# Kernel optimization log

Hardware: AMD Instinct MI355X
Metric: run time of the kernel (lower is better)

Reference implementation:

```python
import jax, jax.numpy as jnp
import numpy as np
from jax import lax

SIGMA = 5
RADIUS = int(4 * SIGMA + 0.5)  # 20 -> kernel size 41, pad_size = 41//2 = 20 = RADIUS
D_AP = 2.27
D_DV = 2.27


def _gauss_d1_kernel():
    # gaussian_kernel1d(sigma, order=1, radius): q(x) = -x/sigma^2, kernel = q(x)*phi(x)
    x = np.arange(-RADIUS, RADIUS + 1).astype(np.float64)
    phi = np.exp(-0.5 / SIGMA ** 2 * x ** 2)
    phi = phi / phi.sum()
    return ((-x / SIGMA ** 2) * phi).astype(np.float32)

_KERNEL = jnp.asarray(_gauss_d1_kernel())


def _conv1d_valid(x, k):
    # x: [N, L], k: [K] -> [N, L-K+1]; cross-correlation, same as torch F.conv1d
    return lax.conv_general_dilated(x[:, None, :], k[None, None, :], (1,), 'VALID')[:, 0, :]


def diffY(x):
    # circular padding along H, derivative / dDV
    c, h, w = x.shape
    xp = jnp.pad(x, ((0, 0), (RADIUS, RADIUS), (0, 0)), mode='wrap')
    xp = jnp.transpose(xp, (0, 2, 1)).reshape(c * w, h + 2 * RADIUS)
    out = _conv1d_valid(xp, _KERNEL).reshape(c, w, h)
    return jnp.transpose(out, (0, 2, 1)) / D_DV


def diffX(x):
    # reflect padding along W, derivative / dAP
    c, h, w = x.shape
    xp = jnp.pad(x, ((0, 0), (0, 0), (RADIUS, RADIUS)), mode='reflect')
    out = _conv1d_valid(xp.reshape(c * h, w + 2 * RADIUS), _KERNEL).reshape(c, h, w)
    return out / D_AP


def setup_inputs() -> dict:
    key = jax.random.key(0)
    k1, k2, k3, k4, k5 = jax.random.split(key, 5)
    H, W = 1024, 2048
    return {
        'y': jax.random.normal(k1, (5, H, W), dtype=jnp.float32),
        'v': jax.random.normal(k2, (2, H, W), dtype=jnp.float32),
        'gamma_ds': jax.random.normal(k3, (H, W), dtype=jnp.float32),
        'cad_coefs': jax.random.uniform(k4, (3,), dtype=jnp.float32),
        'myo_coefs': jax.random.uniform(k5, (5,), dtype=jnp.float32),
    }


def reference(y, v, gamma_ds, cad_coefs, myo_coefs):
    H, W = y.shape[-2:]
    m4 = y[:4]                                  # [4,H,W] myosin components
    c1 = y[4:]                                  # [1,H,W] cadherin

    d1_m = jnp.stack([diffY(m4), diffX(m4)], axis=-1).reshape(2, 2, H, W, 2)
    m = m4.reshape(2, 2, H, W)
    d1_c = jnp.stack([diffY(c1), diffX(c1)], axis=-1).reshape(H, W, 2)
    c = c1[0]

    d1_v = jnp.stack([diffY(v), diffX(v)], axis=-1)   # [2,H,W,2]: d1_v[i,y,x,j] = d_j v_i
    gv = jnp.einsum('iyxj->ijyx', d1_v)
    gvT = jnp.einsum('jyxi->ijyx', d1_v)
    O = -0.5 * (gv - gvT)                       # vorticity
    E = 0.5 * (gv + gvT)                        # strain rate

    eye = jnp.eye(2, dtype=y.dtype)[:, :, None, None]
    trm_yx = jnp.einsum('kkyx->yx', m)
    deviatoric = m - 0.5 * trm_yx[None, None] * eye

    m_norm = jnp.sqrt(jnp.sum(m * m, axis=(0, 1), keepdims=True))            # [1,1,H,W]
    m_0 = jnp.mean(m_norm, axis=(2, 3), keepdims=True)                       # [1,1,1,1]
    dev_mag = jnp.sqrt(jnp.sum(deviatoric * deviatoric, axis=(0, 1), keepdims=True))
    devE = jnp.einsum('klyx,klyx->yx', deviatoric, E)[None, None]

    E_active = E - jnp.sign(devE) * devE * deviatoric / dev_mag ** 2
    E_active = 0.5 * E_active * dev_mag / m_0
    E_passive = E - E_active

    mE = (jnp.einsum('ikyx,kjyx->ijyx', m, E_passive)
          + jnp.einsum('ikyx,kjyx->ijyx', E_passive, m))

    cad = jax.nn.relu(cad_coefs)
    myo = jax.nn.relu(myo_coefs)

    cdot = (-jnp.einsum('iyx,yxi->yx', v, d1_c)
            - cad[0] * c
            + cad[1] * c * jnp.einsum('iyxi->yx', d1_v)
            + cad[2] * gamma_ds)

    trm = trm_yx[None, None]
    gamma_dv = jnp.array([[1.0, 0.0], [0.0, 0.0]], dtype=y.dtype)[:, :, None, None]

    mdot = (-jnp.einsum('kyx,ijyxk->ijyx', v, d1_m)
            - jnp.einsum('ikyx,kjyx->ijyx', O, m)
            + jnp.einsum('ikyx,kjyx->ijyx', m, O)
            - myo[0] * m
            + myo[1] * mE
            - myo[2] * c[None, None] * mE
            + myo[3] * trm * gamma_dv
            + myo[4] * trm * m)

    return jnp.concatenate([mdot.reshape(4, H, W), cdot[None]], axis=0)
```

## Files before the change

kernel.cpp:

```cpp
#include <hip/hip_runtime.h>
#include <math.h>

#define RAD 20
#define KLEN 41
#define NH 1024
#define NW 2048
#define NHW (NH * NW)

struct KW { float w[KLEN]; };
constexpr double cexp_neg(double u) {
  double term = 1.0, sum = 1.0;
  for (int k = 1; k < 30; ++k) { term *= (-u) / (double)k; sum += term; }
  return sum;
}
constexpr KW make_kw() {
  KW r{};
  double ph[KLEN] = {};
  double s = 0.0;
  for (int i = 0; i < KLEN; ++i) {
    double d = (double)(i - RAD);
    double e = cexp_neg(d * d / 800.0);
    e = e * e; e = e * e; e = e * e; e = e * e;
    ph[i] = e; s += e;
  }
  for (int i = 0; i < KLEN; ++i) {
    double d = (double)(i - RAD);
    r.w[i] = (float)((-d / 25.0) * (ph[i] / s) / 2.27);
  }
  return r;
}
static constexpr KW KWC = make_kw();

template <int K>
__device__ __forceinline__ void tap(float s, float& r0, float& r1, float& r2,
                                    float& r3, float& r4, float& r5, float& r6,
                                    float& r7) {
  if constexpr (K - 0 >= 0 && K - 0 <= 40) r0 = fmaf(s, KWC.w[K - 0], r0);
  if constexpr (K - 1 >= 0 && K - 1 <= 40) r1 = fmaf(s, KWC.w[K - 1], r1);
  if constexpr (K - 2 >= 0 && K - 2 <= 40) r2 = fmaf(s, KWC.w[K - 2], r2);
  if constexpr (K - 3 >= 0 && K - 3 <= 40) r3 = fmaf(s, KWC.w[K - 3], r3);
  if constexpr (K - 4 >= 0 && K - 4 <= 40) r4 = fmaf(s, KWC.w[K - 4], r4);
  if constexpr (K - 5 >= 0 && K - 5 <= 40) r5 = fmaf(s, KWC.w[K - 5], r5);
  if constexpr (K - 6 >= 0 && K - 6 <= 40) r6 = fmaf(s, KWC.w[K - 6], r6);
  if constexpr (K - 7 >= 0 && K - 7 <= 40) r7 = fmaf(s, KWC.w[K - 7], r7);
}

#define R8 r0, r1, r2, r3, r4, r5, r6, r7

#define TW 64
#define TH 32
#define TILE_CH ((TH + 2 * RAD) * TW)

__device__ __forceinline__ void conv_col(const float* __restrict__ t, int base,
                                         int lane, float& r0, float& r1,
                                         float& r2, float& r3, float& r4,
                                         float& r5, float& r6, float& r7) {
#define CCHUNK(c)                                      \
  {                                                    \
    float s0 = t[(base + 4 * (c) + 0) * TW + lane];    \
    float s1 = t[(base + 4 * (c) + 1) * TW + lane];    \
    float s2 = t[(base + 4 * (c) + 2) * TW + lane];    \
    float s3 = t[(base + 4 * (c) + 3) * TW + lane];    \
    tap<4 * (c) + 0>(s0, R8);                          \
    tap<4 * (c) + 1>(s1, R8);                          \
    tap<4 * (c) + 2>(s2, R8);                          \
    tap<4 * (c) + 3>(s3, R8);                          \
  }
  CCHUNK(0) CCHUNK(1) CCHUNK(2) CCHUNK(3) CCHUNK(4) CCHUNK(5)
  CCHUNK(6) CCHUNK(7) CCHUNK(8) CCHUNK(9) CCHUNK(10) CCHUNK(11)
#undef CCHUNK
}

__global__ __launch_bounds__(256) void k_reduce(const float* __restrict__ y,
                                                double* __restrict__ acc) {
  const int tid = blockIdx.x * blockDim.x + threadIdx.x;
  const int stride = gridDim.x * blockDim.x;
  double local = 0.0;
  for (int q = tid; q < NHW / 4; q += stride) {
    float4 a = ((const float4*)y)[q];
    float4 b = ((const float4*)(y + NHW))[q];
    float4 c = ((const float4*)(y + 2 * (size_t)NHW))[q];
    float4 d = ((const float4*)(y + 3 * (size_t)NHW))[q];
    local += (double)sqrtf(a.x * a.x + b.x * b.x + c.x * c.x + d.x * d.x);
    local += (double)sqrtf(a.y * a.y + b.y * b.y + c.y * c.y + d.y * d.y);
    local += (double)sqrtf(a.z * a.z + b.z * b.z + c.z * c.z + d.z * d.z);
    local += (double)sqrtf(a.w * a.w + b.w * b.w + c.w * c.w + d.w * d.w);
  }
#pragma unroll
  for (int off = 32; off > 0; off >>= 1) local += __shfl_down(local, off, 64);
  __shared__ double smem[4];
  const int lane = threadIdx.x & 63;
  const int wid = threadIdx.x >> 6;
  if (lane == 0) smem[wid] = local;
  __syncthreads();
  if (threadIdx.x == 0) {
    double s = smem[0] + smem[1] + smem[2] + smem[3];
    atomicAdd(acc, s);
  }
}

__global__ __launch_bounds__(256) void k_dx(const float* __restrict__ y,
                                            const float* __restrict__ v,
                                            float* __restrict__ ws) {
  __shared__ float row[2120];
  const int t = threadIdx.x;
  const int r = blockIdx.x;
  const int ch = blockIdx.y;
  const float* src = (ch < 5) ? (y + (size_t)ch * NHW) : (v + (size_t)(ch - 5) * NHW);
  const float* rp = src + (size_t)r * NW;

#define SWZ(i) ((i) + ((i) >> 6))
#define ST(i, val) { const int ii_ = (i); row[SWZ(ii_)] = (val); }

  const float4* rp4 = (const float4*)rp;
  float4 b0 = rp4[t];
  float4 b1 = rp4[t + 256];
  ST(RAD + 4 * t + 0, b0.x)
  ST(RAD + 4 * t + 1, b0.y)
  ST(RAD + 4 * t + 2, b0.z)
  ST(RAD + 4 * t + 3, b0.w)
  ST(RAD + 4 * (t + 256) + 0, b1.x)
  ST(RAD + 4 * (t + 256) + 1, b1.y)
  ST(RAD + 4 * (t + 256) + 2, b1.z)
  ST(RAD + 4 * (t + 256) + 3, b1.w)
  if (t < RAD) {
    ST(t, rp[RAD - t])
    ST(NW + RAD + t, rp[NW - 2 - t])
  }
  __syncthreads();

  const int xb = 8 * t;
  float r0 = 0.f, r1 = 0.f, r2 = 0.f, r3 = 0.f;
  float r4 = 0.f, r5 = 0.f, r6 = 0.f, r7 = 0.f;
#define RD(k) { const int x_ = xb + (k); float s_ = row[SWZ(x_)]; tap<(k)>(s_, R8); }
  RD(0)  RD(1)  RD(2)  RD(3)  RD(4)  RD(5)  RD(6)  RD(7)
  RD(8)  RD(9)  RD(10) RD(11) RD(12) RD(13) RD(14) RD(15)
  RD(16) RD(17) RD(18) RD(19) RD(20) RD(21) RD(22) RD(23)
  RD(24) RD(25) RD(26) RD(27) RD(28) RD(29) RD(30) RD(31)
  RD(32) RD(33) RD(34) RD(35) RD(36) RD(37) RD(38) RD(39)
  RD(40) RD(41) RD(42) RD(43) RD(44) RD(45) RD(46) RD(47)
#undef RD

  float4 o0, o1;
  o0.x = r0; o0.y = r1; o0.z = r2; o0.w = r3;
  o1.x = r4; o1.y = r5; o1.z = r6; o1.w = r7;
  float4* dst = (float4*)(ws + (size_t)(7 + ch) * NHW + (size_t)r * NW + xb);
  dst[0] = o0;
  dst[1] = o1;
}

__global__ __launch_bounds__(256, 4) void k_dyf(
    const float* __restrict__ y, const float* __restrict__ v,
    const float* __restrict__ gds, const float* __restrict__ cadc,
    const float* __restrict__ myoc, const float* __restrict__ ws,
    const double* __restrict__ acc, float* __restrict__ out) {
  __shared__ float tile[2 * TILE_CH];
  const int lane = threadIdx.x & 63;
  const int wid = threadIdx.x >> 6;
  const int x0 = blockIdx.x * TW;
  const int yb = blockIdx.y * TH;
  const int base = wid * 8;

  const float m0 = (float)(acc[0] / (double)NHW);
  const float cad0 = fmaxf(cadc[0], 0.f);
  const float cad1 = fmaxf(cadc[1], 0.f);
  const float cad2 = fmaxf(cadc[2], 0.f);
  const float my0 = fmaxf(myoc[0], 0.f);
  const float my1 = fmaxf(myoc[1], 0.f);
  const float my2 = fmaxf(myoc[2], 0.f);
  const float my3 = fmaxf(myoc[3], 0.f);
  const float my4 = fmaxf(myoc[4], 0.f);

#define SGLD(sp, k) \
  (sp)[(size_t)(((yb - RAD + wid + 4 * (k)) + NH) & (NH - 1)) * NW + x0 + lane]

  float u0, u1, u2, u3, u4, u5, u6, u7, u8;
  float u9, u10, u11, u12, u13, u14, u15, u16, u17;

#define LOADCH(srcp)                                                   \
  {                                                                    \
    const float* sp_ = (srcp);                                         \
    u0 = SGLD(sp_, 0); u1 = SGLD(sp_, 1); u2 = SGLD(sp_, 2);           \
    u3 = SGLD(sp_, 3); u4 = SGLD(sp_, 4); u5 = SGLD(sp_, 5);           \
    u6 = SGLD(sp_, 6); u7 = SGLD(sp_, 7); u8 = SGLD(sp_, 8);           \
    u9 = SGLD(sp_, 9); u10 = SGLD(sp_, 10); u11 = SGLD(sp_, 11);       \
    u12 = SGLD(sp_, 12); u13 = SGLD(sp_, 13); u14 = SGLD(sp_, 14);     \
    u15 = SGLD(sp_, 15); u16 = SGLD(sp_, 16); u17 = SGLD(sp_, 17);     \
  }
#define WRITECH(g)                                                        \
  {                                                                       \
    float* tb_ = &tile[(g) * TILE_CH];                                    \
    tb_[(wid + 0) * TW + lane] = u0;   tb_[(wid + 4) * TW + lane] = u1;   \
    tb_[(wid + 8) * TW + lane] = u2;   tb_[(wid + 12) * TW + lane] = u3;  \
    tb_[(wid + 16) * TW + lane] = u4;  tb_[(wid + 20) * TW + lane] = u5;  \
    tb_[(wid + 24) * TW + lane] = u6;  tb_[(wid + 28) * TW + lane] = u7;  \
    tb_[(wid + 32) * TW + lane] = u8;  tb_[(wid + 36) * TW + lane] = u9;  \
    tb_[(wid + 40) * TW + lane] = u10; tb_[(wid + 44) * TW + lane] = u11; \
    tb_[(wid + 48) * TW + lane] = u12; tb_[(wid + 52) * TW + lane] = u13; \
    tb_[(wid + 56) * TW + lane] = u14; tb_[(wid + 60) * TW + lane] = u15; \
    tb_[(wid + 64) * TW + lane] = u16; tb_[(wid + 68) * TW + lane] = u17; \
  }
#define DECL8(P)                                                       \
  float P##0 = 0.f, P##1 = 0.f, P##2 = 0.f, P##3 = 0.f, P##4 = 0.f,    \
        P##5 = 0.f, P##6 = 0.f, P##7 = 0.f;
#define CALLCONV(g, P)                                                  \
  conv_col(&tile[(g) * TILE_CH], base, lane, P##0, P##1, P##2, P##3,    \
           P##4, P##5, P##6, P##7);

  DECL8(ym00) DECL8(ym01) DECL8(ym10) DECL8(ym11)
  DECL8(yc) DECL8(yv0) DECL8(yv1)

  LOADCH(y)
  WRITECH(0)
  __syncthreads();
  LOADCH(y + (size_t)NHW)
  CALLCONV(0, ym00)
  WRITECH(1)
  __syncthreads();
  LOADCH(y + 2 * (size_t)NHW)
  CALLCONV(1, ym01)
  WRITECH(0)
  __syncthreads();
  LOADCH(y + 3 * (size_t)NHW)
  CALLCONV(0, ym10)
  WRITECH(1)
  __syncthreads();
  LOADCH(y + 4 * (size_t)NHW)
  CALLCONV(1, ym11)
  WRITECH(0)
  __syncthreads();
  LOADCH(v)
  CALLCONV(0, yc)
  WRITECH(1)
  __syncthreads();
  LOADCH(v + (size_t)NHW)
  CALLCONV(1, yv0)
  WRITECH(0)
  __syncthreads();
  CALLCONV(0, yv1)

#define POINT(q)                                                              \
  {                                                                           \
    const size_t idx = (size_t)(yb + base + (q)) * NW + x0 + lane;            \
    const float m00 = y[idx];                                                 \
    const float m01 = y[idx + (size_t)NHW];                                   \
    const float m10 = y[idx + 2 * (size_t)NHW];                               \
    const float m11 = y[idx + 3 * (size_t)NHW];                               \
    const float c = y[idx + 4 * (size_t)NHW];                                 \
    const float v0 = v[idx];                                                  \
    const float v1 = v[idx + (size_t)NHW];                                    \
    const float g = gds[idx];                                                 \
    const float dY_m00 = ym00##q, dY_m01 = ym01##q;                           \
    const float dY_m10 = ym10##q, dY_m11 = ym11##q;                           \
    const float dY_c = yc##q, dY_v0 = yv0##q, dY_v1 = yv1##q;                 \
    const float dX_m00 = ws[idx + 7 * (size_t)NHW];                           \
    const float dX_m01 = ws[idx + 8 * (size_t)NHW];                           \
    const float dX_m10 = ws[idx + 9 * (size_t)NHW];                           \
    const float dX_m11 = ws[idx + 10 * (size_t)NHW];                          \
    const float dX_c = ws[idx + 11 * (size_t)NHW];                            \
    const float dX_v0 = ws[idx + 12 * (size_t)NHW];                           \
    const float dX_v1 = ws[idx + 13 * (size_t)NHW];                           \
    const float gv00 = dY_v0, gv01 = dX_v0, gv10 = dY_v1, gv11 = dX_v1;       \
    const float ww = -0.5f * (gv01 - gv10);                                   \
    const float E00 = gv00, E11 = gv11;                                       \
    const float E01 = 0.5f * (gv01 + gv10);                                   \
    const float E10 = E01;                                                    \
    const float trm = m00 + m11;                                              \
    const float dev00 = m00 - 0.5f * trm;                                     \
    const float dev01 = m01;                                                  \
    const float dev10 = m10;                                                  \
    const float dev11 = m11 - 0.5f * trm;                                     \
    const float dmag_sq =                                                     \
        dev00 * dev00 + dev01 * dev01 + dev10 * dev10 + dev11 * dev11;        \
    const float dm = sqrtf(dmag_sq);                                          \
    const float dm2 = dm * dm;                                                \
    const float devE = dev00 * E00 + dev01 * E01 + dev10 * E10 + dev11 * E11; \
    const float sg = (devE > 0.f) ? 1.f : ((devE < 0.f) ? -1.f : 0.f);        \
    const float coef = sg * devE / dm2;                                       \
    const float sc = 0.5f * dm / m0;                                          \
    const float Ea00 = (E00 - coef * dev00) * sc;                             \
    const float Ea01 = (E01 - coef * dev01) * sc;                             \
    const float Ea10 = (E10 - coef * dev10) * sc;                             \
    const float Ea11 = (E11 - coef * dev11) * sc;                             \
    const float Ep00 = E00 - Ea00;                                            \
    const float Ep01 = E01 - Ea01;                                            \
    const float Ep10 = E10 - Ea10;                                            \
    const float Ep11 = E11 - Ea11;                                            \
    const float mE00 = (m00 * Ep00 + m01 * Ep10) + (Ep00 * m00 + Ep01 * m10); \
    const float mE01 = (m00 * Ep01 + m01 * Ep11) + (Ep00 * m01 + Ep01 * m11); \
    const float mE10 = (m10 * Ep00 + m11 * Ep10) + (Ep10 * m00 + Ep11 * m10); \
    const float mE11 = (m10 * Ep01 + m11 * Ep11) + (Ep10 * m01 + Ep11 * m11); \
    const float divv = gv00 + gv11;                                           \
    const float cdot =                                                        \
        -(v0 * dY_c + v1 * dX_c) - cad0 * c + cad1 * c * divv + cad2 * g;     \
    const float md00 = -(v0 * dY_m00 + v1 * dX_m00) - ww * m10 - ww * m01 -   \
                       my0 * m00 + my1 * mE00 - my2 * c * mE00 + my3 * trm +  \
                       my4 * trm * m00;                                       \
    const float md01 = -(v0 * dY_m01 + v1 * dX_m01) - ww * m11 + ww * m00 -   \
                       my0 * m01 + my1 * mE01 - my2 * c * mE01 +              \
                       my4 * trm * m01;                                       \
    const float md10 = -(v0 * dY_m10 + v1 * dX_m10) + ww * m00 - ww * m11 -   \
                       my0 * m10 + my1 * mE10 - my2 * c * mE10 +              \
                       my4 * trm * m10;                                       \
    const float md11 = -(v0 * dY_m11 + v1 * dX_m11) + ww * m01 + ww * m10 -   \
                       my0 * m11 + my1 * mE11 - my2 * c * mE11 +              \
                       my4 * trm * m11;                                       \
    out[idx] = md00;                                                          \
    out[idx + (size_t)NHW] = md01;                                            \
    out[idx + 2 * (size_t)NHW] = md10;                                        \
    out[idx + 3 * (size_t)NHW] = md11;                                        \
    out[idx + 4 * (size_t)NHW] = cdot;                                        \
  }

  POINT(0) POINT(1) POINT(2) POINT(3)
  POINT(4) POINT(5) POINT(6) POINT(7)
#undef POINT
}

extern "C" void kernel_launch(void* const* d_in, const int* in_sizes, int n_in,
                              void* d_out, int out_size, void* d_ws, size_t ws_size,
                              hipStream_t stream) {
  (void)in_sizes; (void)n_in; (void)out_size; (void)ws_size;
  const float* y = (const float*)d_in[0];
  const float* v = (const float*)d_in[1];
  const float* gds = (const float*)d_in[2];
  const float* cadc = (const float*)d_in[3];
  const float* myoc = (const float*)d_in[4];
  float* out = (float*)d_out;

  double* acc = (double*)d_ws;
  float* planes = (float*)((char*)d_ws + 512);

  hipMemsetAsync(acc, 0, sizeof(double), stream);
  k_reduce<<<dim3(1024), dim3(256), 0, stream>>>(y, acc);
  k_dx<<<dim3(NH, 7), dim3(256), 0, stream>>>(y, v, planes);
  k_dyf<<<dim3(NW / TW, NH / TH), dim3(256), 0, stream>>>(y, v, gds, cadc, myoc,
                                                          planes, acc, out);
}
```

Baseline: 179.6 us.

## Fuse myosin-magnitude reduction into dx kernel and vectorize dy tile loads

Removes the separate k_reduce launch. The channel-0 blocks of k_dx now load the other three myosin rows and compute the sqrt-magnitude reduction, reusing the row already in registers. Separately, k_dyf's halo tile load is changed from scalar per-lane loads to float4 loads and stores spread across the block. The fusion adds load imbalance: channel-0 blocks do four times the reads plus an extra barrier and atomic. The float4 tile writes may change the LDS bank pattern.

```diff
diff --git a/kernel.cpp b/kernel.cpp
--- a/kernel.cpp
+++ b/kernel.cpp
@@ -71,38 +71,12 @@
 #undef CCHUNK
 }
 
-__global__ __launch_bounds__(256) void k_reduce(const float* __restrict__ y,
-                                                double* __restrict__ acc) {
-  const int tid = blockIdx.x * blockDim.x + threadIdx.x;
-  const int stride = gridDim.x * blockDim.x;
-  double local = 0.0;
-  for (int q = tid; q < NHW / 4; q += stride) {
-    float4 a = ((const float4*)y)[q];
-    float4 b = ((const float4*)(y + NHW))[q];
-    float4 c = ((const float4*)(y + 2 * (size_t)NHW))[q];
-    float4 d = ((const float4*)(y + 3 * (size_t)NHW))[q];
-    local += (double)sqrtf(a.x * a.x + b.x * b.x + c.x * c.x + d.x * d.x);
-    local += (double)sqrtf(a.y * a.y + b.y * b.y + c.y * c.y + d.y * d.y);
-    local += (double)sqrtf(a.z * a.z + b.z * b.z + c.z * c.z + d.z * d.z);
-    local += (double)sqrtf(a.w * a.w + b.w * b.w + c.w * c.w + d.w * d.w);
-  }
-#pragma unroll
-  for (int off = 32; off > 0; off >>= 1) local += __shfl_down(local, off, 64);
-  __shared__ double smem[4];
-  const int lane = threadIdx.x & 63;
-  const int wid = threadIdx.x >> 6;
-  if (lane == 0) smem[wid] = local;
-  __syncthreads();
-  if (threadIdx.x == 0) {
-    double s = smem[0] + smem[1] + smem[2] + smem[3];
-    atomicAdd(acc, s);
-  }
-}
-
 __global__ __launch_bounds__(256) void k_dx(const float* __restrict__ y,
                                             const float* __restrict__ v,
-                                            float* __restrict__ ws) {
+                                            float* __restrict__ ws,
+                                            double* __restrict__ acc) {
   __shared__ float row[2120];
+  __shared__ double rsm[4];
   const int t = threadIdx.x;
   const int r = blockIdx.x;
   const int ch = blockIdx.y;
@@ -115,6 +89,17 @@
   const float4* rp4 = (const float4*)rp;
   float4 b0 = rp4[t];
   float4 b1 = rp4[t + 256];
+
+  float4 a1x, a1y, a2x, a2y, a3x, a3y;
+  if (ch == 0) {
+    const float4* p1 = (const float4*)(y + (size_t)NHW + (size_t)r * NW);
+    const float4* p2 = (const float4*)(y + 2 * (size_t)NHW + (size_t)r * NW);
+    const float4* p3 = (const float4*)(y + 3 * (size_t)NHW + (size_t)r * NW);
+    a1x = p1[t]; a1y = p1[t + 256];
+    a2x = p2[t]; a2y = p2[t + 256];
+    a3x = p3[t]; a3y = p3[t + 256];
+  }
+
   ST(RAD + 4 * t + 0, b0.x)
   ST(RAD + 4 * t + 1, b0.y)
   ST(RAD + 4 * t + 2, b0.z)
@@ -147,6 +132,25 @@
   float4* dst = (float4*)(ws + (size_t)(7 + ch) * NHW + (size_t)r * NW + xb);
   dst[0] = o0;
   dst[1] = o1;
+
+  if (ch == 0) {
+    double local =
+        (double)sqrtf(b0.x * b0.x + a1x.x * a1x.x + a2x.x * a2x.x + a3x.x * a3x.x) +
+        (double)sqrtf(b0.y * b0.y + a1x.y * a1x.y + a2x.y * a2x.y + a3x.y * a3x.y) +
+        (double)sqrtf(b0.z * b0.z + a1x.z * a1x.z + a2x.z * a2x.z + a3x.z * a3x.z) +
+        (double)sqrtf(b0.w * b0.w + a1x.w * a1x.w + a2x.w * a2x.w + a3x.w * a3x.w) +
+        (double)sqrtf(b1.x * b1.x + a1y.x * a1y.x + a2y.x * a2y.x + a3y.x * a3y.x) +
+        (double)sqrtf(b1.y * b1.y + a1y.y * a1y.y + a2y.y * a2y.y + a3y.y * a3y.y) +
+        (double)sqrtf(b1.z * b1.z + a1y.z * a1y.z + a2y.z * a2y.z + a3y.z * a3y.z) +
+        (double)sqrtf(b1.w * b1.w + a1y.w * a1y.w + a2y.w * a2y.w + a3y.w * a3y.w);
+#pragma unroll
+    for (int off = 32; off > 0; off >>= 1) local += __shfl_down(local, off, 64);
+    const int lane = t & 63;
+    const int wid = t >> 6;
+    if (lane == 0) rsm[wid] = local;
+    __syncthreads();
+    if (t == 0) atomicAdd(acc, rsm[0] + rsm[1] + rsm[2] + rsm[3]);
+  }
 }
 
 __global__ __launch_bounds__(256, 4) void k_dyf(
@@ -157,6 +161,7 @@
   __shared__ float tile[2 * TILE_CH];
   const int lane = threadIdx.x & 63;
   const int wid = threadIdx.x >> 6;
+  const int t = threadIdx.x;
   const int x0 = blockIdx.x * TW;
   const int yb = blockIdx.y * TH;
   const int base = wid * 8;
@@ -171,34 +176,34 @@
   const float my3 = fmaxf(myoc[3], 0.f);
   const float my4 = fmaxf(myoc[4], 0.f);
 
-#define SGLD(sp, k) \
-  (sp)[(size_t)(((yb - RAD + wid + 4 * (k)) + NH) & (NH - 1)) * NW + x0 + lane]
-
-  float u0, u1, u2, u3, u4, u5, u6, u7, u8;
-  float u9, u10, u11, u12, u13, u14, u15, u16, u17;
-
-#define LOADCH(srcp)                                                   \
-  {                                                                    \
-    const float* sp_ = (srcp);                                         \
-    u0 = SGLD(sp_, 0); u1 = SGLD(sp_, 1); u2 = SGLD(sp_, 2);           \
-    u3 = SGLD(sp_, 3); u4 = SGLD(sp_, 4); u5 = SGLD(sp_, 5);           \
-    u6 = SGLD(sp_, 6); u7 = SGLD(sp_, 7); u8 = SGLD(sp_, 8);           \
-    u9 = SGLD(sp_, 9); u10 = SGLD(sp_, 10); u11 = SGLD(sp_, 11);       \
-    u12 = SGLD(sp_, 12); u13 = SGLD(sp_, 13); u14 = SGLD(sp_, 14);     \
-    u15 = SGLD(sp_, 15); u16 = SGLD(sp_, 16); u17 = SGLD(sp_, 17);     \
-  }
-#define WRITECH(g)                                                        \
-  {                                                                       \
-    float* tb_ = &tile[(g) * TILE_CH];                                    \
-    tb_[(wid + 0) * TW + lane] = u0;   tb_[(wid + 4) * TW + lane] = u1;   \
-    tb_[(wid + 8) * TW + lane] = u2;   tb_[(wid + 12) * TW + lane] = u3;  \
-    tb_[(wid + 16) * TW + lane] = u4;  tb_[(wid + 20) * TW + lane] = u5;  \
-    tb_[(wid + 24) * TW + lane] = u6;  tb_[(wid + 28) * TW + lane] = u7;  \
-    tb_[(wid + 32) * TW + lane] = u8;  tb_[(wid + 36) * TW + lane] = u9;  \
-    tb_[(wid + 40) * TW + lane] = u10; tb_[(wid + 44) * TW + lane] = u11; \
-    tb_[(wid + 48) * TW + lane] = u12; tb_[(wid + 52) * TW + lane] = u13; \
-    tb_[(wid + 56) * TW + lane] = u14; tb_[(wid + 60) * TW + lane] = u15; \
-    tb_[(wid + 64) * TW + lane] = u16; tb_[(wid + 68) * TW + lane] = u17; \
+  float4 f40, f41, f42, f43, f44;
+#define LD4Q(dst, q_, sp_)                                                  \
+  {                                                                         \
+    const int q = (q_);                                                     \
+    const int row_ = q >> 4;                                                \
+    const int c4_ = (q & 15) * 4;                                           \
+    const int wr_ = ((yb - RAD + row_) + NH) & (NH - 1);                    \
+    dst = *(const float4*)((sp_) + (size_t)wr_ * NW + x0 + c4_);            \
+  }
+#define LOADCH(srcp)                                                        \
+  {                                                                         \
+    const float* sp_ = (srcp);                                              \
+    LD4Q(f40, t, sp_) LD4Q(f41, t + 256, sp_) LD4Q(f42, t + 512, sp_)       \
+    LD4Q(f43, t + 768, sp_)                                                 \
+    if (t < 128) { LD4Q(f44, t + 1024, sp_) }                               \
+  }
+#define WR4Q(src, q_, g)                                                    \
+  {                                                                         \
+    const int q = (q_);                                                     \
+    const int row_ = q >> 4;                                                \
+    const int c4_ = (q & 15) * 4;                                           \
+    *(float4*)&tile[(g) * TILE_CH + row_ * TW + c4_] = src;                 \
+  }
+#define WRITECH(g)                                                          \
+  {                                                                         \
+    WR4Q(f40, t, g) WR4Q(f41, t + 256, g) WR4Q(f42, t + 512, g)             \
+    WR4Q(f43, t + 768, g)                                                   \
+    if (t < 128) { WR4Q(f44, t + 1024, g) }                                 \
   }
 #define DECL8(P)                                                       \
   float P##0 = 0.f, P##1 = 0.f, P##2 = 0.f, P##3 = 0.f, P##4 = 0.f,    \
@@ -332,8 +337,7 @@
   float* planes = (float*)((char*)d_ws + 512);
 
   hipMemsetAsync(acc, 0, sizeof(double), stream);
-  k_reduce<<<dim3(1024), dim3(256), 0, stream>>>(y, acc);
-  k_dx<<<dim3(NH, 7), dim3(256), 0, stream>>>(y, v, planes);
+  k_dx<<<dim3(NH, 7), dim3(256), 0, stream>>>(y, v, planes, acc);
   k_dyf<<<dim3(NW / TW, NH / TH), dim3(256), 0, stream>>>(y, v, gds, cadc, myoc,
                                                           planes, acc, out);
 }
```

Result: slower. 255.0 us (+42.0%).
